# Kernel optimization log

Measured on AMD Instinct MI355X. Metric: run time of the kernel, lower is better.

The kernel has to match this reference:

```python
import jax, jax.numpy as jnp
import numpy as np

N_AGENTS = 32
STATE_DIM = 2048
EMBED = 64
BS, T = 64, 32


def setup_inputs() -> dict:
    key = jax.random.key(0)
    ks = jax.random.split(key, 12)
    def lin(k, fan_in, fan_out):
        return jax.random.normal(k, (fan_in, fan_out), dtype=jnp.float32) / np.sqrt(fan_in)
    return {
        "agent_qs": jax.random.normal(ks[0], (BS, T, N_AGENTS), dtype=jnp.float32),
        "states": jax.random.normal(ks[1], (BS, T, STATE_DIM), dtype=jnp.float32),
        "Ww1": lin(ks[2], STATE_DIM, EMBED * N_AGENTS),
        "bw1": jnp.zeros((EMBED * N_AGENTS,), jnp.float32),
        "Wwf": lin(ks[3], STATE_DIM, EMBED),
        "bwf": jnp.zeros((EMBED,), jnp.float32),
        "Wb1": lin(ks[4], STATE_DIM, EMBED),
        "bb1": jnp.zeros((EMBED,), jnp.float32),
        "Wv1": lin(ks[5], STATE_DIM, EMBED),
        "bv1": jnp.zeros((EMBED,), jnp.float32),
        "Wv2": lin(ks[6], EMBED, 1),
        "bv2": jnp.zeros((1,), jnp.float32),
    }


def _mix(qs, st, Ww1, bw1, Wwf, bwf, Wb1, bb1, Wv1, bv1, Wv2, bv2):
    # qs: [B,1,A], st: [B,S] -> q_tot [B]
    w1 = jnp.abs(st @ Ww1 + bw1).reshape(-1, N_AGENTS, EMBED)          # [B,A,E]
    b1 = (st @ Wb1 + bb1)[:, None, :]                                   # [B,1,E]
    hidden = jax.nn.elu(jnp.einsum('bia,bae->bie', qs, w1) + b1)        # [B,1,E]
    w_final = jnp.abs(st @ Wwf + bwf)                                   # [B,E]
    v = jax.nn.relu(st @ Wv1 + bv1) @ Wv2 + bv2                         # [B,1]
    y = jnp.einsum('bie,be->bi', hidden, w_final) + v                   # [B,1]
    return y[:, 0]


def reference(agent_qs, states, Ww1, bw1, Wwf, bwf, Wb1, bb1, Wv1, bv1, Wv2, bv2):
    bs = agent_qs.shape[0]
    st = states.reshape(-1, STATE_DIM)                   # [B,S]
    qs = agent_qs.reshape(-1, 1, N_AGENTS)               # [B,1,A]
    B = st.shape[0]
    params = (Ww1, bw1, Wwf, bwf, Wb1, bb1, Wv1, bv1, Wv2, bv2)

    # --- wc_calculate (fully detached) ---
    q_tot = _mix(qs, st, *params)                        # [B]
    dim2 = STATE_DIM // N_AGENTS
    st3 = st.reshape(B, N_AGENTS, dim2)
    mask = 1.0 - jnp.eye(N_AGENTS, dtype=st.dtype)       # [A,A]: row i zeros agent-i chunk
    masked = (st3[None, :, :, :] * mask[:, None, :, None]).reshape(N_AGENTS * B, STATE_DIM)
    qs_rep = jnp.broadcast_to(qs[None], (N_AGENTS, B, 1, N_AGENTS)).reshape(N_AGENTS * B, 1, N_AGENTS)
    q1 = _mix(qs_rep, masked, *params).reshape(N_AGENTS, B)
    wc = jnp.abs(q_tot[None, :] - q1).T                  # [B,A]
    wc = wc / jnp.maximum(jnp.linalg.norm(wc, axis=1, keepdims=True), 1e-12)
    wc = jax.lax.stop_gradient(wc)[:, None, :]           # [B,1,A]

    # --- final mix with importance-weighted qs ---
    q_tot_final = _mix(qs * wc, st, *params)             # [B]
    return q_tot_final.reshape(bs, -1, 1)
```

## Files before the change

kernel.cpp:

```cpp
#include <hip/hip_runtime.h>
#include <math.h>
#include <stdint.h>

#define NA 32
#define SD 2048
#define BT 2048
#define NFRG 144

typedef float floatx4 __attribute__((ext_vector_type(4)));
typedef short bf16x8  __attribute__((ext_vector_type(8)));

__device__ __forceinline__ unsigned short f2bf(float f) {
    union { float f; uint32_t u; } v; v.f = f;
    uint32_t r = v.u + 0x7FFFu + ((v.u >> 16) & 1u);
    return (unsigned short)(r >> 16);
}


__global__ __launch_bounds__(256) void k0_ast(const float* __restrict__ st,
                                              unsigned short* __restrict__ stA) {
    int idx = blockIdx.x * 256 + threadIdx.x;
    int m = idx >> 8, kg = idx & 255;
    int k0 = kg * 8;
    const float* src = st + (size_t)m * SD + k0;
    float4 v0 = *(const float4*)src;
    float4 v1 = *(const float4*)(src + 4);
    int bt = m >> 4, l16 = m & 15, kc = kg >> 2, quad = kg & 3;
    unsigned short* dst = stA + ((size_t)bt * 64 + kc) * 512 + (quad * 16 + l16) * 8;
    ushort4 o0, o1;
    o0.x = f2bf(v0.x); o0.y = f2bf(v0.y); o0.z = f2bf(v0.z); o0.w = f2bf(v0.w);
    o1.x = f2bf(v1.x); o1.y = f2bf(v1.y); o1.z = f2bf(v1.z); o1.w = f2bf(v1.w);
    *(ushort4*)(dst)     = o0;
    *(ushort4*)(dst + 4) = o1;
}

__global__ __launch_bounds__(256) void k0_wswz(const float* __restrict__ Ww1,
                                               const float* __restrict__ Wwf,
                                               const float* __restrict__ Wb1,
                                               const float* __restrict__ Wv1,
                                               unsigned short* __restrict__ Wswz) {
    __shared__ float tile[32][33];
    const int n0 = blockIdx.x * 32;
    const int k0 = blockIdx.y * 32;
    const float* src; int ld = 64, nb = 0;
    if (n0 < 2048)      { src = Ww1; ld = 2048; nb = n0; }
    else if (n0 < 2112) { src = Wwf; nb = n0 - 2048; }
    else if (n0 < 2176) { src = Wb1; nb = n0 - 2112; }
    else if (n0 < 2240) { src = Wv1; nb = n0 - 2176; }
    else                { src = nullptr; }
    const int t = threadIdx.x;
    {
        int nl = t & 31, kl0 = t >> 5;
        #pragma unroll
        for (int r = 0; r < 4; r++) {
            int kl = kl0 + r * 8;
            tile[kl][nl] = src ? src[(size_t)(k0 + kl) * ld + nb + nl] : 0.f;
        }
    }
    __syncthreads();
    {
        int kl = t & 31, nl0 = t >> 5;
        #pragma unroll
        for (int r = 0; r < 4; r++) {
            int nl = nl0 + r * 8;
            int n = n0 + nl, k = k0 + kl;
            int f = n >> 4, l16 = n & 15;
            int i = k >> 6, kr = k & 63;
            int h = kr >> 5, quad = (kr & 31) >> 3, j = kr & 7;
            size_t off = (((size_t)i * NFRG + f) * 2 + h) * 512 + (quad * 16 + l16) * 8 + j;
            Wswz[off] = f2bf(tile[kl][nl]);
        }
    }
}

__global__ void k0_bias(const float* __restrict__ bw1, const float* __restrict__ bwf,
                        const float* __restrict__ bb1, const float* __restrict__ bv1,
                        float* __restrict__ bcat) {
    int n = blockIdx.x * 256 + threadIdx.x;
    if (n >= NFRG * 16) return;
    float v = 0.f;
    if (n < 2048)      v = bw1[n];
    else if (n < 2112) v = bwf[n - 2048];
    else if (n < 2176) v = bb1[n - 2112];
    else if (n < 2240) v = bv1[n - 2176];
    bcat[n] = v;
}

__global__ __launch_bounds__(256) void k1_gemm(const unsigned short* __restrict__ stA,
                                               const unsigned short* __restrict__ Wswz,
                                               const float* __restrict__ bcat,
                                               float* __restrict__ Ycn)
{
    const int t = threadIdx.x;
    const int m0t = blockIdx.x * 4;
    const int n0f = blockIdx.y * 8;
    const int wid = t >> 6, lane = t & 63;
    const int wm = wid & 1, wn = wid >> 1;
    const int l16 = lane & 15;

    floatx4 acc[2][4];
    #pragma unroll
    for (int i = 0; i < 2; i++)
        #pragma unroll
        for (int j = 0; j < 4; j++) acc[i][j] = (floatx4)0.f;

    const unsigned short* Ap0 = stA + ((size_t)(m0t + wm * 2 + 0) * 64) * 512 + lane * 8;
    const unsigned short* Ap1 = stA + ((size_t)(m0t + wm * 2 + 1) * 64) * 512 + lane * 8;

    #pragma unroll 2
    for (int kc = 0; kc < 64; kc++) {
        bf16x8 a0 = *(const bf16x8*)(Ap0 + (size_t)kc * 512);
        bf16x8 a1 = *(const bf16x8*)(Ap1 + (size_t)kc * 512);
        const int i = kc >> 1, h = kc & 1;
        const unsigned short* Bp =
            Wswz + (((size_t)i * NFRG + n0f + wn * 4) * 2 + h) * 512 + lane * 8;
        #pragma unroll
        for (int nf = 0; nf < 4; nf++) {
            bf16x8 b = *(const bf16x8*)(Bp + (size_t)nf * 1024);
            acc[0][nf] = __builtin_amdgcn_mfma_f32_16x16x32_bf16(a0, b, acc[0][nf], 0, 0, 0);
            acc[1][nf] = __builtin_amdgcn_mfma_f32_16x16x32_bf16(a1, b, acc[1][nf], 0, 0, 0);
        }
    }

    #pragma unroll
    for (int mf = 0; mf < 2; mf++)
        #pragma unroll
        for (int nf = 0; nf < 4; nf++) {
            const int f  = n0f + wn * 4 + nf;
            const int bt = m0t + wm * 2 + mf;
            const float bias = bcat[f * 16 + l16];
            floatx4 o;
            #pragma unroll
            for (int r = 0; r < 4; r++) o[r] = -(acc[mf][nf][r] + bias);
            *(floatx4*)(Ycn + ((size_t)bt * NFRG + f) * 256 + lane * 4) = o;
        }
}

__global__ __launch_bounds__(64) void k3_q1(
    const unsigned short* __restrict__ stA, const float* __restrict__ qs,
    const unsigned short* __restrict__ Wswz, const float* __restrict__ Wv2,
    const float* __restrict__ bv2, const float* __restrict__ Ycn,
    float* __restrict__ q1)
{
    const int bt = blockIdx.x;
    const int i  = blockIdx.y;
    __shared__ float qs_s[16][33];

    const int t = threadIdx.x;
    const int quad = t >> 4, l16 = t & 15;

    {
        int b = t >> 2, a0 = (t & 3) * 8;
        const float* src = qs + (size_t)(bt * 16 + b) * NA + a0;
        #pragma unroll
        for (int u = 0; u < 8; u++) qs_s[b][a0 + u] = src[u];
    }
    bf16x8 A0 = *(const bf16x8*)(stA + ((size_t)bt * 64 + 2 * i + 0) * 512 + t * 8);
    bf16x8 A1 = *(const bf16x8*)(stA + ((size_t)bt * 64 + 2 * i + 1) * 512 + t * 8);
    __syncthreads();

    floatx4 hid[4];
    #pragma unroll
    for (int nf = 0; nf < 4; nf++) hid[nf] = (floatx4)0.f;

    const float*          Yb = Ycn  + (size_t)bt * NFRG * 256;
    const unsigned short* Wb = Wswz + (size_t)i * NFRG * 1024;

    for (int a = 0; a < 32; a++) {
        const float*          yp = Yb + (size_t)(a * 4) * 256 + t * 4;
        const unsigned short* wp = Wb + (size_t)(a * 4) * 1024 + t * 8;
        floatx4 acc[4];
        #pragma unroll
        for (int nf = 0; nf < 4; nf++) acc[nf] = *(const floatx4*)(yp + nf * 256);
        #pragma unroll
        for (int nf = 0; nf < 4; nf++) {
            bf16x8 b0 = *(const bf16x8*)(wp + nf * 1024);
            bf16x8 b1 = *(const bf16x8*)(wp + nf * 1024 + 512);
            acc[nf] = __builtin_amdgcn_mfma_f32_16x16x32_bf16(A0, b0, acc[nf], 0, 0, 0);
            acc[nf] = __builtin_amdgcn_mfma_f32_16x16x32_bf16(A1, b1, acc[nf], 0, 0, 0);
        }
        float qv[4];
        #pragma unroll
        for (int r = 0; r < 4; r++) qv[r] = qs_s[quad * 4 + r][a];
        #pragma unroll
        for (int nf = 0; nf < 4; nf++)
            #pragma unroll
            for (int r = 0; r < 4; r++)
                hid[nf][r] += qv[r] * fabsf(acc[nf][r]);
    }

    floatx4 wff[4], b1f[4], vacc = (floatx4)0.f;
    #pragma unroll
    for (int nft = 0; nft < 12; nft++) {
        const int f = 128 + nft;
        floatx4 c = *(const floatx4*)(Yb + (size_t)f * 256 + t * 4);
        const unsigned short* wp = Wb + (size_t)f * 1024 + t * 8;
        c = __builtin_amdgcn_mfma_f32_16x16x32_bf16(A0, *(const bf16x8*)(wp),       c, 0, 0, 0);
        c = __builtin_amdgcn_mfma_f32_16x16x32_bf16(A1, *(const bf16x8*)(wp + 512), c, 0, 0, 0);
        if (nft < 4) {
            #pragma unroll
            for (int r = 0; r < 4; r++) wff[nft][r] = fabsf(c[r]);
        } else if (nft < 8) {
            #pragma unroll
            for (int r = 0; r < 4; r++) b1f[nft - 4][r] = -c[r];
        } else {
            float wv2 = Wv2[(nft - 8) * 16 + l16];
            #pragma unroll
            for (int r = 0; r < 4; r++) vacc[r] += fmaxf(-c[r], 0.f) * wv2;
        }
    }

    const float bv2v = bv2[0];
    #pragma unroll
    for (int r = 0; r < 4; r++) {
        float s = vacc[r];
        #pragma unroll
        for (int nf = 0; nf < 4; nf++) {
            float h = hid[nf][r] + b1f[nf][r];
            h = h > 0.f ? h : expm1f(h);
            s += h * wff[nf][r];
        }
        s += __shfl_xor(s, 1); s += __shfl_xor(s, 2);
        s += __shfl_xor(s, 4); s += __shfl_xor(s, 8);
        if (l16 == 0) q1[(size_t)i * BT + bt * 16 + quad * 4 + r] = s + bv2v;
    }
}

__global__ __launch_bounds__(256) void k4_final(
    const float* __restrict__ qs, const float* __restrict__ Ycn,
    const float* __restrict__ q1, const float* __restrict__ Wv2,
    const float* __restrict__ bv2, float* __restrict__ out)
{
    const int bt = blockIdx.x;
    __shared__ float qs_s[16][33];
    __shared__ float qw_s[16][33];
    __shared__ float hidp[4][16][64];
    __shared__ float wfb[16][64], b1b[16][64], vb[16][64];
    __shared__ float qt[16];

    const int t = threadIdx.x, w = t >> 6, lane = t & 63;
    const int quad = lane >> 4, l16 = lane & 15;
    const float bv2v = bv2[0];

    {
        int l = t * 2;
        float2 v = *(const float2*)&qs[(size_t)(bt * 16 + (l >> 5)) * NA + (l & 31)];
        qs_s[l >> 5][(l & 31) + 0] = v.x;
        qs_s[l >> 5][(l & 31) + 1] = v.y;
    }
    __syncthreads();

    const float* Yb = Ycn + (size_t)bt * NFRG * 256;

    floatx4 hid[4];
    #pragma unroll
    for (int nf = 0; nf < 4; nf++) hid[nf] = (floatx4)0.f;
    for (int ia = 0; ia < 8; ia++) {
        const int a = w * 8 + ia;
        const float* yp = Yb + (size_t)(a * 4) * 256 + lane * 4;
        float qv[4];
        #pragma unroll
        for (int r = 0; r < 4; r++) qv[r] = qs_s[quad * 4 + r][a];
        #pragma unroll
        for (int nf = 0; nf < 4; nf++) {
            floatx4 c = *(const floatx4*)(yp + nf * 256);
            #pragma unroll
            for (int r = 0; r < 4; r++) hid[nf][r] += qv[r] * fabsf(c[r]);
        }
    }
    #pragma unroll
    for (int nf = 0; nf < 4; nf++)
        #pragma unroll
        for (int r = 0; r < 4; r++)
            hidp[w][quad * 4 + r][nf * 16 + l16] = hid[nf][r];

    #pragma unroll
    for (int fi = 0; fi < 3; fi++) {
        const int nft = w * 3 + fi;
        floatx4 c = *(const floatx4*)(Yb + (size_t)(128 + nft) * 256 + lane * 4);
        const int e = (nft & 3) * 16 + l16;
        #pragma unroll
        for (int r = 0; r < 4; r++) {
            int b = quad * 4 + r;
            if (nft < 4)      wfb[b][e] = fabsf(c[r]);
            else if (nft < 8) b1b[b][e] = -c[r];
            else              vb[b][e]  = fmaxf(-c[r], 0.f) * Wv2[e];
        }
    }
    __syncthreads();

    #pragma unroll
    for (int bb = 0; bb < 4; bb++) {
        int b = w * 4 + bb;
        float h = hidp[0][b][lane] + hidp[1][b][lane]
                + hidp[2][b][lane] + hidp[3][b][lane] + b1b[b][lane];
        h = h > 0.f ? h : expm1f(h);
        float val = h * wfb[b][lane] + vb[b][lane];
        #pragma unroll
        for (int off = 32; off > 0; off >>= 1) val += __shfl_xor(val, off);
        if (lane == 0) qt[b] = val + bv2v;
    }
    __syncthreads();

    {
        const int rr = w * 4 + quad;
        float qtv = qt[rr];
        float d0 = fabsf(qtv - q1[(size_t)(2 * l16 + 0) * BT + bt * 16 + rr]);
        float d1 = fabsf(qtv - q1[(size_t)(2 * l16 + 1) * BT + bt * 16 + rr]);
        float ss = d0 * d0 + d1 * d1;
        ss += __shfl_xor(ss, 1); ss += __shfl_xor(ss, 2);
        ss += __shfl_xor(ss, 4); ss += __shfl_xor(ss, 8);
        float inv = 1.f / fmaxf(sqrtf(ss), 1e-12f);
        qw_s[rr][2 * l16 + 0] = qs_s[rr][2 * l16 + 0] * d0 * inv;
        qw_s[rr][2 * l16 + 1] = qs_s[rr][2 * l16 + 1] * d1 * inv;
    }
    __syncthreads();

    floatx4 hid2[4];
    #pragma unroll
    for (int nf = 0; nf < 4; nf++) hid2[nf] = (floatx4)0.f;
    for (int ia = 0; ia < 8; ia++) {
        const int a = w * 8 + ia;
        const float* yp = Yb + (size_t)(a * 4) * 256 + lane * 4;
        float qv[4];
        #pragma unroll
        for (int r = 0; r < 4; r++) qv[r] = qw_s[quad * 4 + r][a];
        #pragma unroll
        for (int nf = 0; nf < 4; nf++) {
            floatx4 c = *(const floatx4*)(yp + nf * 256);
            #pragma unroll
            for (int r = 0; r < 4; r++) hid2[nf][r] += qv[r] * fabsf(c[r]);
        }
    }
    #pragma unroll
    for (int nf = 0; nf < 4; nf++)
        #pragma unroll
        for (int r = 0; r < 4; r++)
            hidp[w][quad * 4 + r][nf * 16 + l16] = hid2[nf][r];
    __syncthreads();

    #pragma unroll
    for (int bb = 0; bb < 4; bb++) {
        int b = w * 4 + bb;
        float h = hidp[0][b][lane] + hidp[1][b][lane]
                + hidp[2][b][lane] + hidp[3][b][lane] + b1b[b][lane];
        h = h > 0.f ? h : expm1f(h);
        float val = h * wfb[b][lane] + vb[b][lane];
        #pragma unroll
        for (int off = 32; off > 0; off >>= 1) val += __shfl_xor(val, off);
        if (lane == 0) out[bt * 16 + b] = val + bv2v;
    }
}

extern "C" void kernel_launch(void* const* d_in, const int* in_sizes, int n_in,
                              void* d_out, int out_size, void* d_ws, size_t ws_size,
                              hipStream_t stream) {
    const float* qs  = (const float*)d_in[0];
    const float* st  = (const float*)d_in[1];
    const float* Ww1 = (const float*)d_in[2];
    const float* bw1 = (const float*)d_in[3];
    const float* Wwf = (const float*)d_in[4];
    const float* bwf = (const float*)d_in[5];
    const float* Wb1 = (const float*)d_in[6];
    const float* bb1 = (const float*)d_in[7];
    const float* Wv1 = (const float*)d_in[8];
    const float* bv1 = (const float*)d_in[9];
    const float* Wv2 = (const float*)d_in[10];
    const float* bv2 = (const float*)d_in[11];
    float* out = (float*)d_out;

    float* Ycn           = (float*)d_ws;
    unsigned short* stA  = (unsigned short*)(Ycn + (size_t)128 * NFRG * 256);
    unsigned short* Wswz = stA + (size_t)SD * SD;
    float* bcat          = (float*)(Wswz + (size_t)32 * NFRG * 1024);
    float* q1v           = bcat + NFRG * 16;

    k0_ast <<<(SD * SD / 8 + 255) / 256, 256, 0, stream>>>(st, stA);
    k0_wswz<<<dim3(NFRG / 2, SD / 32), 256, 0, stream>>>(Ww1, Wwf, Wb1, Wv1, Wswz);
    k0_bias<<<(NFRG * 16 + 255) / 256, 256, 0, stream>>>(bw1, bwf, bb1, bv1, bcat);

    k1_gemm<<<dim3(BT / 64, NFRG / 8), 256, 0, stream>>>(stA, Wswz, bcat, Ycn);
    k3_q1  <<<dim3(BT / 16, NA), 64, 0, stream>>>(stA, qs, Wswz, Wv2, bv2, Ycn, q1v);
    k4_final<<<BT / 16, 256, 0, stream>>>(qs, Ycn, q1v, Wv2, bv2, out);
}
```

Measured before the change: 217.9 us.

## Software-pipeline GEMM operand loads and pack four waves per q1 block

The main GEMM loop now double-buffers its A and B fragments in registers, loading the next k-chunk while the MFMAs for the current chunk issue, so global load latency overlaps with compute. The q1 kernel moves from 64-thread single-wave blocks to 256-thread blocks holding four independent waves, each with its own slice of shared qs storage. This cuts the block count fourfold and may improve scheduling and occupancy. The prefetch adds register pressure, and the unrolled loop is now a plain loop.

```diff
diff --git a/kernel.cpp b/kernel.cpp
--- a/kernel.cpp
+++ b/kernel.cpp
@@ -106,20 +106,35 @@
 
     const unsigned short* Ap0 = stA + ((size_t)(m0t + wm * 2 + 0) * 64) * 512 + lane * 8;
     const unsigned short* Ap1 = stA + ((size_t)(m0t + wm * 2 + 1) * 64) * 512 + lane * 8;
-
-    #pragma unroll 2
+    const unsigned short* Bbase = Wswz + ((size_t)(n0f + wn * 4) * 2) * 512 + lane * 8;
+
+    bf16x8 a0c = *(const bf16x8*)(Ap0);
+    bf16x8 a1c = *(const bf16x8*)(Ap1);
+    bf16x8 bc[4];
+    #pragma unroll
+    for (int nf = 0; nf < 4; nf++)
+        bc[nf] = *(const bf16x8*)(Bbase + (size_t)nf * 1024);
+
     for (int kc = 0; kc < 64; kc++) {
-        bf16x8 a0 = *(const bf16x8*)(Ap0 + (size_t)kc * 512);
-        bf16x8 a1 = *(const bf16x8*)(Ap1 + (size_t)kc * 512);
-        const int i = kc >> 1, h = kc & 1;
-        const unsigned short* Bp =
-            Wswz + (((size_t)i * NFRG + n0f + wn * 4) * 2 + h) * 512 + lane * 8;
-        #pragma unroll
-        for (int nf = 0; nf < 4; nf++) {
-            bf16x8 b = *(const bf16x8*)(Bp + (size_t)nf * 1024);
-            acc[0][nf] = __builtin_amdgcn_mfma_f32_16x16x32_bf16(a0, b, acc[0][nf], 0, 0, 0);
-            acc[1][nf] = __builtin_amdgcn_mfma_f32_16x16x32_bf16(a1, b, acc[1][nf], 0, 0, 0);
-        }
+        bf16x8 a0n, a1n, bn[4];
+        if (kc < 63) {
+            const int kn = kc + 1;
+            a0n = *(const bf16x8*)(Ap0 + (size_t)kn * 512);
+            a1n = *(const bf16x8*)(Ap1 + (size_t)kn * 512);
+            const unsigned short* Bp =
+                Bbase + ((size_t)(kn >> 1) * NFRG * 2 + (kn & 1)) * 512;
+            #pragma unroll
+            for (int nf = 0; nf < 4; nf++)
+                bn[nf] = *(const bf16x8*)(Bp + (size_t)nf * 1024);
+        }
+        #pragma unroll
+        for (int nf = 0; nf < 4; nf++) {
+            acc[0][nf] = __builtin_amdgcn_mfma_f32_16x16x32_bf16(a0c, bc[nf], acc[0][nf], 0, 0, 0);
+            acc[1][nf] = __builtin_amdgcn_mfma_f32_16x16x32_bf16(a1c, bc[nf], acc[1][nf], 0, 0, 0);
+        }
+        a0c = a0n; a1c = a1n;
+        #pragma unroll
+        for (int nf = 0; nf < 4; nf++) bc[nf] = bn[nf];
     }
 
     #pragma unroll
@@ -136,27 +151,28 @@
         }
 }
 
-__global__ __launch_bounds__(64) void k3_q1(
+__global__ __launch_bounds__(256) void k3_q1(
     const unsigned short* __restrict__ stA, const float* __restrict__ qs,
     const unsigned short* __restrict__ Wswz, const float* __restrict__ Wv2,
     const float* __restrict__ bv2, const float* __restrict__ Ycn,
     float* __restrict__ q1)
 {
-    const int bt = blockIdx.x;
     const int i  = blockIdx.y;
-    __shared__ float qs_s[16][33];
-
-    const int t = threadIdx.x;
-    const int quad = t >> 4, l16 = t & 15;
+    const int t  = threadIdx.x;
+    const int w  = t >> 6, lane = t & 63;
+    const int bt = blockIdx.x * 4 + w;
+    const int quad = lane >> 4, l16 = lane & 15;
+
+    __shared__ float qs_s[4][16][33];
 
     {
-        int b = t >> 2, a0 = (t & 3) * 8;
+        int b = lane >> 2, a0 = (lane & 3) * 8;
         const float* src = qs + (size_t)(bt * 16 + b) * NA + a0;
         #pragma unroll
-        for (int u = 0; u < 8; u++) qs_s[b][a0 + u] = src[u];
-    }
-    bf16x8 A0 = *(const bf16x8*)(stA + ((size_t)bt * 64 + 2 * i + 0) * 512 + t * 8);
-    bf16x8 A1 = *(const bf16x8*)(stA + ((size_t)bt * 64 + 2 * i + 1) * 512 + t * 8);
+        for (int u = 0; u < 8; u++) qs_s[w][b][a0 + u] = src[u];
+    }
+    bf16x8 A0 = *(const bf16x8*)(stA + ((size_t)bt * 64 + 2 * i + 0) * 512 + lane * 8);
+    bf16x8 A1 = *(const bf16x8*)(stA + ((size_t)bt * 64 + 2 * i + 1) * 512 + lane * 8);
     __syncthreads();
 
     floatx4 hid[4];
@@ -167,8 +183,8 @@
     const unsigned short* Wb = Wswz + (size_t)i * NFRG * 1024;
 
     for (int a = 0; a < 32; a++) {
-        const float*          yp = Yb + (size_t)(a * 4) * 256 + t * 4;
-        const unsigned short* wp = Wb + (size_t)(a * 4) * 1024 + t * 8;
+        const float*          yp = Yb + (size_t)(a * 4) * 256 + lane * 4;
+        const unsigned short* wp = Wb + (size_t)(a * 4) * 1024 + lane * 8;
         floatx4 acc[4];
         #pragma unroll
         for (int nf = 0; nf < 4; nf++) acc[nf] = *(const floatx4*)(yp + nf * 256);
@@ -181,7 +197,7 @@
         }
         float qv[4];
         #pragma unroll
-        for (int r = 0; r < 4; r++) qv[r] = qs_s[quad * 4 + r][a];
+        for (int r = 0; r < 4; r++) qv[r] = qs_s[w][quad * 4 + r][a];
         #pragma unroll
         for (int nf = 0; nf < 4; nf++)
             #pragma unroll
@@ -193,8 +209,8 @@
     #pragma unroll
     for (int nft = 0; nft < 12; nft++) {
         const int f = 128 + nft;
-        floatx4 c = *(const floatx4*)(Yb + (size_t)f * 256 + t * 4);
-        const unsigned short* wp = Wb + (size_t)f * 1024 + t * 8;
+        floatx4 c = *(const floatx4*)(Yb + (size_t)f * 256 + lane * 4);
+        const unsigned short* wp = Wb + (size_t)f * 1024 + lane * 8;
         c = __builtin_amdgcn_mfma_f32_16x16x32_bf16(A0, *(const bf16x8*)(wp),       c, 0, 0, 0);
         c = __builtin_amdgcn_mfma_f32_16x16x32_bf16(A1, *(const bf16x8*)(wp + 512), c, 0, 0, 0);
         if (nft < 4) {
@@ -380,6 +396,6 @@
     k0_bias<<<(NFRG * 16 + 255) / 256, 256, 0, stream>>>(bw1, bwf, bb1, bv1, bcat);
 
     k1_gemm<<<dim3(BT / 64, NFRG / 8), 256, 0, stream>>>(stA, Wswz, bcat, Ycn);
-    k3_q1  <<<dim3(BT / 16, NA), 64, 0, stream>>>(stA, qs, Wswz, Wv2, bv2, Ycn, q1v);
+    k3_q1  <<<dim3(BT / 64, NA), 256, 0, stream>>>(stA, qs, Wswz, Wv2, bv2, Ycn, q1v);
     k4_final<<<BT / 16, 256, 0, stream>>>(qs, Ycn, q1v, Wv2, bv2, out);
 }
```

Result: slower. 259.0 us (+18.8%).
